# Kernel tuning notes

Measured on AMD Instinct MI355X. Metric: run time of the kernel, lower is better.

Reference implementation:

```python
import jax, jax.numpy as jnp
import numpy as np

N_NODES = 100000
N_EDGES = 1280000
IN_DIM = 64
HID = 64
OUT_DIM = 2
N_GRAPHS = 1000
BN_EPS = 1e-5


def setup_inputs() -> dict:
    key = jax.random.key(0)
    ks = jax.random.split(key, 16)
    x = jax.random.normal(ks[0], (N_NODES, IN_DIM), dtype=jnp.float32)
    edge_index = jax.random.randint(ks[1], (2, N_EDGES), 0, N_NODES, dtype=jnp.int64)
    batch = jnp.sort(jax.random.randint(ks[2], (N_NODES,), 0, N_GRAPHS, dtype=jnp.int64))
    # He-init linear weights (stored as [in, out] so forward is x @ W)
    def he(k, fan_in, fan_out):
        return jax.random.normal(k, (fan_in, fan_out), dtype=jnp.float32) * np.sqrt(2.0 / fan_in)
    return {
        "x": x,
        "edge_index": edge_index,
        "batch": batch,
        "bn_in_g": jnp.ones((IN_DIM,), jnp.float32),
        "bn_in_b": jnp.zeros((IN_DIM,), jnp.float32),
        "W1": he(ks[3], IN_DIM, HID), "b1": jnp.zeros((HID,), jnp.float32),
        "g1": jnp.ones((HID,), jnp.float32), "be1": jnp.zeros((HID,), jnp.float32),
        "W2": he(ks[4], HID, HID), "b2": jnp.zeros((HID,), jnp.float32),
        "g2": jnp.ones((HID,), jnp.float32), "be2": jnp.zeros((HID,), jnp.float32),
        "Wout": he(ks[5], HID, OUT_DIM), "bout": jnp.zeros((OUT_DIM,), jnp.float32),
    }


def _batchnorm(x, g, b):
    # training-mode BN over the node dimension (biased variance, as torch uses for normalization)
    m = jnp.mean(x, axis=0)
    v = jnp.mean(jnp.square(x - m), axis=0)
    return (x - m) * jax.lax.rsqrt(v + BN_EPS) * g + b


def _gcn_norm(edge_index, n):
    # PyG GCNConv normalization with added self-loops:
    # norm_e = deg[src]^-1/2 * deg[dst]^-1/2, deg computed on A + I over targets.
    row = jnp.concatenate([edge_index[0], jnp.arange(n, dtype=edge_index.dtype)])
    col = jnp.concatenate([edge_index[1], jnp.arange(n, dtype=edge_index.dtype)])
    deg = jax.ops.segment_sum(jnp.ones_like(col, dtype=jnp.float32), col, num_segments=n)
    dinv = jnp.where(deg > 0, jax.lax.rsqrt(deg), 0.0)
    norm = dinv[row] * dinv[col]
    return row, col, norm


def _gcn_conv(x, W, b, row, col, norm, n):
    h = x @ W                                   # [N, out]
    msg = h[row] * norm[:, None]                # gather over edges (incl. self-loops)
    agg = jax.ops.segment_sum(msg, col, num_segments=n)
    return agg + b


def reference(x, edge_index, batch, bn_in_g, bn_in_b, W1, b1, g1, be1, W2, b2, g2, be2, Wout, bout):
    n = x.shape[0]
    row, col, norm = _gcn_norm(edge_index, n)
    h = _batchnorm(x, bn_in_g, bn_in_b)         # input BN (dropout = identity in eval)
    h = _gcn_conv(h, W1, b1, row, col, norm, n)
    h = _batchnorm(jax.nn.relu(h), g1, be1)
    h = _gcn_conv(h, W2, b2, row, col, norm, n)
    h = _batchnorm(jax.nn.relu(h), g2, be2)
    # global mean pool per graph
    sums = jax.ops.segment_sum(h, batch, num_segments=N_GRAPHS)
    cnts = jax.ops.segment_sum(jnp.ones((n,), h.dtype), batch, num_segments=N_GRAPHS)
    pooled = sums / jnp.maximum(cnts, 1.0)[:, None]
    return pooled @ Wout + bout                 # [N_GRAPHS, OUT_DIM]
```

## Files before the change

kernel.cpp:

```cpp
#include <hip/hip_runtime.h>
#include <math.h>

#define N_NODES 100000
#define N_EDGES 1280000
#define DIM 64
#define N_GRAPHS 1000
#define BN_EPS 1e-5f
#define NB 392
#define P1B 256
#define P1E 5000
#define SB 400
#define WIN 128
#define NWIN (N_EDGES / WIN)
#define NSLOT 32

__device__ __forceinline__ unsigned int bf16_rtn2(float a, float b) {
    unsigned int ua = __float_as_uint(a);
    unsigned int ub = __float_as_uint(b);
    ua = (ua + 0x7FFFu + ((ua >> 16) & 1u)) >> 16;
    ub = (ub + 0x7FFFu + ((ub >> 16) & 1u)) >> 16;
    return ua | (ub << 16);
}
__device__ __forceinline__ unsigned short bf16r(float a) {
    unsigned int u = __float_as_uint(a);
    return (unsigned short)((u + 0x7FFFu + ((u >> 16) & 1u)) >> 16);
}
__device__ __forceinline__ float bfup(unsigned short u) {
    return __uint_as_float(((unsigned int)u) << 16);
}
__device__ __forceinline__ float blo(unsigned int v) { return __uint_as_float(v << 16); }
__device__ __forceinline__ float bhi(unsigned int v) { return __uint_as_float(v & 0xFFFF0000u); }

__global__ __launch_bounds__(256) void k_p1hist(const int* __restrict__ ei,
                                                const int* __restrict__ batch,
                                                const float* __restrict__ X,
                                                int* __restrict__ bh,
                                                int* __restrict__ start,
                                                float* __restrict__ gsum,
                                                float* __restrict__ gsumsq) {
    int t = threadIdx.x;
    if (blockIdx.x < P1B) {
        __shared__ int hist[NB];
        for (int b = t; b < NB; b += 256) hist[b] = 0;
        __syncthreads();
        int e0 = blockIdx.x * P1E;
        #pragma unroll 4
        for (int e = e0 + t; e < e0 + P1E; e += 256)
            atomicAdd(&hist[ei[N_EDGES + e] >> 8], 1);
        __syncthreads();
        for (int b = t; b < NB; b += 256) bh[b * P1B + blockIdx.x] = hist[b];
    } else if (blockIdx.x < P1B + SB) {
        int grp = blockIdx.x - P1B;
        int j = t & 63, rg = t >> 6;
        int base = grp * 250;
        float s = 0.f, s2 = 0.f;
        for (int i = base + rg; i < base + 250; i += 4) {
            float v = X[i * DIM + j];
            s += v; s2 += v * v;
        }
        __shared__ float ls[256], ls2[256];
        ls[t] = s; ls2[t] = s2;
        __syncthreads();
        if (t < 64) {
            int slot = (grp & (NSLOT - 1)) * DIM;
            s  = ls[j]  + ls[64 + j]  + ls[128 + j]  + ls[192 + j];
            s2 = ls2[j] + ls2[64 + j] + ls2[128 + j] + ls2[192 + j];
            atomicAdd(&gsum[slot + j], s);
            atomicAdd(&gsumsq[slot + j], s2);
        }
    } else {
        int i = (blockIdx.x - P1B - SB) * 256 + t;
        if (i < N_NODES) {
            int cur = batch[i];
            if (i == 0) { for (int q = 0; q <= cur; q++) start[q] = 0; }
            else {
                int prev = batch[i - 1];
                for (int q = prev + 1; q <= cur; q++) start[q] = i;
            }
            if (i == N_NODES - 1)
                for (int q = cur + 1; q <= N_GRAPHS; q++) start[q] = N_NODES;
        }
    }
}

__global__ void k_scan1(const int* __restrict__ bh, int* __restrict__ iscan,
                        int* __restrict__ bsum) {
    __shared__ int ls[256];
    int i = blockIdx.x * 256 + threadIdx.x;
    int v = bh[i];
    ls[threadIdx.x] = v;
    __syncthreads();
    for (int off = 1; off < 256; off <<= 1) {
        int tv = (threadIdx.x >= off) ? ls[threadIdx.x - off] : 0;
        __syncthreads();
        ls[threadIdx.x] += tv;
        __syncthreads();
    }
    iscan[i] = ls[threadIdx.x];
    if (threadIdx.x == 255) bsum[blockIdx.x] = ls[255];
}

__global__ void k_scan2(const int* __restrict__ bsum, int* __restrict__ boff) {
    __shared__ int ls[512];
    int t = threadIdx.x;
    int v0 = (t < NB) ? bsum[t] : 0;
    ls[t] = v0;
    __syncthreads();
    for (int off = 1; off < 512; off <<= 1) {
        int v = (t >= off) ? ls[t - off] : 0;
        __syncthreads();
        ls[t] += v;
        __syncthreads();
    }
    if (t < NB) boff[t] = ls[t] - v0;
}

__global__ __launch_bounds__(256) void k_p1scat(const int* __restrict__ ei,
                                                const int* __restrict__ bh,
                                                const int* __restrict__ iscan,
                                                const int* __restrict__ boff,
                                                int* __restrict__ tmp) {
    __shared__ int cur[NB];
    int blk = blockIdx.x;
    for (int b = threadIdx.x; b < NB; b += 256) {
        int i = b * P1B + blk;
        cur[b] = boff[b] + iscan[i] - bh[i];
    }
    __syncthreads();
    int e0 = blk * P1E;
    for (int e = e0 + threadIdx.x; e < e0 + P1E; e += 256) {
        int r = ei[e], c = ei[N_EDGES + e];
        int pos = atomicAdd(&cur[c >> 8], 1);
        tmp[pos] = (r << 8) | (c & 255);
    }
}

__global__ __launch_bounds__(256) void k_p2a(const int* __restrict__ tmp,
                                             const int* __restrict__ bh,
                                             const int* __restrict__ iscan,
                                             const int* __restrict__ boff,
                                             int* __restrict__ rowstart,
                                             float* __restrict__ dinv,
                                             int* __restrict__ winnode,
                                             float* __restrict__ C) {
    int b = blockIdx.x, t = threadIdx.x;
    int bstart = boff[b] + iscan[b * 256] - bh[b * 256];
    int bend = (b == NB - 1) ? N_EDGES
                             : (boff[b + 1] + iscan[(b + 1) * 256] - bh[(b + 1) * 256]);
    __shared__ int cnt[256], scn[256];
    cnt[t] = 0;
    __syncthreads();
    for (int e = bstart + t; e < bend; e += 256)
        atomicAdd(&cnt[tmp[e] & 255], 1);
    __syncthreads();
    scn[t] = cnt[t];
    __syncthreads();
    for (int off = 1; off < 256; off <<= 1) {
        int v = (t >= off) ? scn[t - off] : 0;
        __syncthreads();
        scn[t] += v;
        __syncthreads();
    }
    int node = b * 256 + t;
    int deg = cnt[t];
    int rs = bstart + scn[t] - deg;
    bool span = false;
    if (node <= N_NODES) rowstart[node] = rs;
    if (node == N_NODES) rowstart[node + 1] = rs;
    if (node < N_NODES) {
        dinv[node] = 1.0f / sqrtf((float)(deg + 1));
        int re = rs + deg;
        for (int w = (rs + WIN - 1) / WIN; w * WIN < re; ++w) winnode[w] = node;
        span = (deg > 0) && (rs / WIN != (re - 1) / WIN);
    }
    int lane = t & 63;
    int wbase = b * 256 + (t & ~63);
    unsigned long long m = __ballot(span);
    while (m) {
        int bit = __builtin_ctzll(m);
        m &= m - 1;
        C[(size_t)(wbase + bit) * DIM + lane] = 0.f;
    }
}

__global__ __launch_bounds__(256) void k_p2b(const int* __restrict__ tmp,
                                             const int* __restrict__ bh,
                                             const int* __restrict__ iscan,
                                             const int* __restrict__ boff,
                                             const int* __restrict__ rowstart,
                                             int* __restrict__ csr) {
    int b = blockIdx.x, t = threadIdx.x;
    int bstart = boff[b] + iscan[b * 256] - bh[b * 256];
    int bend = (b == NB - 1) ? N_EDGES
                             : (boff[b + 1] + iscan[(b + 1) * 256] - bh[(b + 1) * 256]);
    __shared__ int curs[256];
    int node = b * 256 + t;
    curs[t] = (node < N_NODES) ? rowstart[node] : 0;
    __syncthreads();
    for (int e = bstart + t; e < bend; e += 256) {
        int rec = tmp[e];
        int pos = atomicAdd(&curs[rec & 255], 1);
        csr[pos] = (int)((unsigned)rec >> 8);
    }
}

__global__ void k_bnfold(float* __restrict__ gsum, float* __restrict__ gsumsq,
                         const float* __restrict__ g, const float* __restrict__ b,
                         const float* __restrict__ W,
                         float* __restrict__ scale, float* __restrict__ cshift) {
    int j = threadIdx.x;
    float ms = 0.f, m2 = 0.f;
    for (int k = 0; k < NSLOT; k++) {
        ms += gsum[k * DIM + j];   gsum[k * DIM + j] = 0.f;
        m2 += gsumsq[k * DIM + j]; gsumsq[k * DIM + j] = 0.f;
    }
    float mean = ms * (1.0f / N_NODES);
    float var  = m2 * (1.0f / N_NODES) - mean * mean;
    float inv  = 1.0f / sqrtf(var + BN_EPS);
    float sc   = g[j] * inv;
    scale[j] = sc;
    __shared__ float shl[64];
    shl[j] = b[j] - mean * sc;
    __syncthreads();
    float s = 0.f;
    for (int k = 0; k < DIM; k++) s += shl[k] * W[k * DIM + j];
    cshift[j] = s;
}

__global__ void k_bnfinal(const float* __restrict__ gsum, const float* __restrict__ gsumsq,
                          const float* __restrict__ g, const float* __restrict__ b,
                          float* __restrict__ scale, float* __restrict__ shift) {
    int j = threadIdx.x;
    float ms = 0.f, m2 = 0.f;
    for (int k = 0; k < NSLOT; k++) { ms += gsum[k * DIM + j]; m2 += gsumsq[k * DIM + j]; }
    float mean = ms * (1.0f / N_NODES);
    float var  = m2 * (1.0f / N_NODES) - mean * mean;
    float inv  = 1.0f / sqrtf(var + BN_EPS);
    float sc   = g[j] * inv;
    scale[j] = sc;
    shift[j] = b[j] - mean * sc;
}

__global__ __launch_bounds__(256) void k_gemm_f32(const float* __restrict__ X,
                                                  const float* __restrict__ W,
                                                  const float* __restrict__ scale,
                                                  const float* __restrict__ cshift,
                                                  const float* __restrict__ dinv,
                                                  unsigned short* __restrict__ T) {
    __shared__ float Wl[64 * 64];
    __shared__ float Al[64 * 65];
    for (int t = threadIdx.x; t < 4096; t += 256) Wl[t] = W[t] * scale[t >> 6];
    int row0 = blockIdx.x * 64;
    for (int t = threadIdx.x; t < 4096; t += 256) {
        int r = t >> 6, k = t & 63;
        int i = row0 + r;
        Al[r * 65 + k] = (i < N_NODES) ? X[(size_t)i * DIM + k] : 0.f;
    }
    __syncthreads();
    int r = threadIdx.x & 63;
    int q = threadIdx.x >> 6;
    float acc[16];
    #pragma unroll
    for (int jj = 0; jj < 16; jj++) acc[jj] = cshift[q * 16 + jj];
    #pragma unroll 4
    for (int k = 0; k < 64; k++) {
        float a = Al[r * 65 + k];
        const float4* wv = (const float4*)&Wl[k * 64 + q * 16];
        float4 w0 = wv[0], w1 = wv[1], w2 = wv[2], w3 = wv[3];
        acc[0]  += a * w0.x; acc[1]  += a * w0.y; acc[2]  += a * w0.z; acc[3]  += a * w0.w;
        acc[4]  += a * w1.x; acc[5]  += a * w1.y; acc[6]  += a * w1.z; acc[7]  += a * w1.w;
        acc[8]  += a * w2.x; acc[9]  += a * w2.y; acc[10] += a * w2.z; acc[11] += a * w2.w;
        acc[12] += a * w3.x; acc[13] += a * w3.y; acc[14] += a * w3.z; acc[15] += a * w3.w;
    }
    int i = row0 + r;
    if (i < N_NODES) {
        float dv = dinv[i];
        unsigned int pk[8];
        #pragma unroll
        for (int jj = 0; jj < 8; jj++)
            pk[jj] = bf16_rtn2(acc[2 * jj] * dv, acc[2 * jj + 1] * dv);
        uint4* outv = (uint4*)&T[(size_t)i * DIM + q * 16];
        outv[0] = make_uint4(pk[0], pk[1], pk[2], pk[3]);
        outv[1] = make_uint4(pk[4], pk[5], pk[6], pk[7]);
    }
}

__global__ __launch_bounds__(256) void k_gemm_b16(const unsigned short* __restrict__ X,
                                                  const float* __restrict__ W,
                                                  const float* __restrict__ scale,
                                                  const float* __restrict__ cshift,
                                                  const float* __restrict__ dinv,
                                                  unsigned short* __restrict__ T) {
    __shared__ float Wl[64 * 64];
    __shared__ float Al[64 * 65];
    for (int t = threadIdx.x; t < 4096; t += 256) Wl[t] = W[t] * scale[t >> 6];
    int row0 = blockIdx.x * 64;
    for (int t = threadIdx.x; t < 4096; t += 256) {
        int r = t >> 6, k = t & 63;
        int i = row0 + r;
        Al[r * 65 + k] = (i < N_NODES) ? bfup(X[(size_t)i * DIM + k]) : 0.f;
    }
    __syncthreads();
    int r = threadIdx.x & 63;
    int q = threadIdx.x >> 6;
    float acc[16];
    #pragma unroll
    for (int jj = 0; jj < 16; jj++) acc[jj] = cshift[q * 16 + jj];
    #pragma unroll 4
    for (int k = 0; k < 64; k++) {
        float a = Al[r * 65 + k];
        const float4* wv = (const float4*)&Wl[k * 64 + q * 16];
        float4 w0 = wv[0], w1 = wv[1], w2 = wv[2], w3 = wv[3];
        acc[0]  += a * w0.x; acc[1]  += a * w0.y; acc[2]  += a * w0.z; acc[3]  += a * w0.w;
        acc[4]  += a * w1.x; acc[5]  += a * w1.y; acc[6]  += a * w1.z; acc[7]  += a * w1.w;
        acc[8]  += a * w2.x; acc[9]  += a * w2.y; acc[10] += a * w2.z; acc[11] += a * w2.w;
        acc[12] += a * w3.x; acc[13] += a * w3.y; acc[14] += a * w3.z; acc[15] += a * w3.w;
    }
    int i = row0 + r;
    if (i < N_NODES) {
        float dv = dinv[i];
        unsigned int pk[8];
        #pragma unroll
        for (int jj = 0; jj < 8; jj++)
            pk[jj] = bf16_rtn2(acc[2 * jj] * dv, acc[2 * jj + 1] * dv);
        uint4* outv = (uint4*)&T[(size_t)i * DIM + q * 16];
        outv[0] = make_uint4(pk[0], pk[1], pk[2], pk[3]);
        outv[1] = make_uint4(pk[4], pk[5], pk[6], pk[7]);
    }
}


#define SWZ(V, S) __builtin_amdgcn_ds_swizzle((V), (((S) << 5) | 0x10))

#define ISSUE(SRCV, TVV, CV, S0) do {                                 \
    SRCV[0] = SWZ(CV, (S0) + 0); SRCV[1] = SWZ(CV, (S0) + 1);         \
    SRCV[2] = SWZ(CV, (S0) + 2); SRCV[3] = SWZ(CV, (S0) + 3);         \
    TVV[0] = T2[(unsigned)SRCV[0] * 16u + cc];                        \
    TVV[1] = T2[(unsigned)SRCV[1] * 16u + cc];                        \
    TVV[2] = T2[(unsigned)SRCV[2] * 16u + cc];                        \
    TVV[3] = T2[(unsigned)SRCV[3] * 16u + cc];                        \
} while (0)

#define STEP(TVV, U, B, FL) do {                                      \
    const int ebs = e0 + 16 * (B) + 4 * (U);                          \
    uint2 tvv = TVV[U];                                               \
    float a0 = blo(tvv.x), a1 = bhi(tvv.x);                           \
    float a2 = blo(tvv.y), a3 = bhi(tvv.y);                           \
    if (re > ebs + 3) {                                               \
        acc0 += a0; acc1 += a1; acc2 += a2; acc3 += a3;               \
    } else {                                                          \
        int lo = ebs;                                                 \
        while (re <= ebs + 3) {                                       \
            int eg = ebs + gg;                                        \
            if (eg >= lo && eg < re) {                                \
                acc0 += a0; acc1 += a1; acc2 += a2; acc3 += a3;       \
            }                                                         \
            lo = re;                                                  \
            FL();                                                     \
        }                                                             \
        if (ebs + gg >= lo) {                                         \
            acc0 += a0; acc1 += a1; acc2 += a2; acc3 += a3;           \
        }                                                             \
    }                                                                 \
} while (0)

#define CONSUME(TVV, B, FL) do {                                      \
    STEP(TVV, 0, B, FL); STEP(TVV, 1, B, FL);                         \
    STEP(TVV, 2, B, FL); STEP(TVV, 3, B, FL);                         \
} while (0)

#define COMB4()                                                       \
    float t0 = acc0 + __shfl_xor(acc0, 16); t0 += __shfl_xor(t0, 32); \
    float t1 = acc1 + __shfl_xor(acc1, 16); t1 += __shfl_xor(t1, 32); \
    float t2 = acc2 + __shfl_xor(acc2, 16); t2 += __shfl_xor(t2, 32); \
    float t3 = acc3 + __shfl_xor(acc3, 16); t3 += __shfl_xor(t3, 32);

#define REDIST64(OUT, V0, V1, V2, V3)                                 \
    float _r0 = __shfl((V0), lane >> 2);                              \
    float _r1 = __shfl((V1), lane >> 2);                              \
    float _r2 = __shfl((V2), lane >> 2);                              \
    float _r3 = __shfl((V3), lane >> 2);                              \
    float OUT = (lane & 2) ? ((lane & 1) ? _r3 : _r2)                 \
                           : ((lane & 1) ? _r1 : _r0);

#define ADVANCE() do {                                                \
    acc0 = acc1 = acc2 = acc3 = 0.f;                                  \
    ++i; ++k;                                                         \
    if (k < 64) re = __builtin_amdgcn_readlane(rsv, k);               \
    else        re = __builtin_amdgcn_readfirstlane(rowstart[i + 1]); \
    tsv = T2[(unsigned)i * 16u + cc];                                 \
} while (0)

#define FLUSH1() do {                                                 \
    COMB4();                                                          \
    if (part) {                                                       \
        REDIST64(cv, t0, t1, t2, t3);                                 \
        atomicAdd(&C[(size_t)i * DIM + lane], cv);                    \
        part = false;                                                 \
    } else {                                                          \
        int cnt = i - i0;                                             \
        float di;                                                     \
        if (cnt < 64)                                                 \
            di = __int_as_float(                                      \
                __builtin_amdgcn_readlane(__float_as_int(dv), cnt));  \
        else di = dinv[i];                                            \
        float h0 = fmaxf((t0 + blo(tsv.x)) * di + bb.x, 0.f);         \
        float h1 = fmaxf((t1 + bhi(tsv.x)) * di + bb.y, 0.f);         \
        float h2 = fmaxf((t2 + blo(tsv.y)) * di + bb.z, 0.f);         \
        float h3 = fmaxf((t3 + bhi(tsv.y)) * di + bb.w, 0.f);         \
        if (lane < 16)                                                \
            ((uint2*)H)[(unsigned)i * 16u + cc] =                     \
                make_uint2(bf16_rtn2(h0, h1), bf16_rtn2(h2, h3));     \
        s0 += h0; s1 += h1; s2 += h2; s3 += h3;                       \
        q0 += h0 * h0; q1 += h1 * h1; q2 += h2 * h2; q3 += h3 * h3;   \
    }                                                                 \
    ADVANCE();                                                        \
} while (0)

__global__ __launch_bounds__(256) void k_gather1(const unsigned short* __restrict__ T,
                                                 const float* __restrict__ dinv,
                                                 const int* __restrict__ rowstart,
                                                 const int* __restrict__ winnode,
                                                 const int* __restrict__ csr,
                                                 const float* __restrict__ bias,
                                                 float* __restrict__ C,
                                                 unsigned short* __restrict__ H,
                                                 float* __restrict__ gsum,
                                                 float* __restrict__ gsumsq) {
    const int lane = threadIdx.x & 63;
    const int gg = lane >> 4;
    const int cc = lane & 15;
    const int w = blockIdx.x * 4 + (threadIdx.x >> 6);
    const int e0 = w * WIN;
    const int eend = e0 + WIN;
    const uint2* T2 = (const uint2*)T;

    int csrv0 = csr[e0 + 4 * cc + gg];
    int csrv1 = csr[e0 + 64 + 4 * cc + gg];
    int i0 = __builtin_amdgcn_readfirstlane(winnode[w]);
    int rsv = rowstart[min(i0 + lane, N_NODES + 1)];
    float dv = dinv[min(i0 + lane, N_NODES - 1)];
    uint2 tsv = T2[(unsigned)i0 * 16u + cc];
    const float4 bb = ((const float4*)bias)[cc];

    int i = i0, k = 1;
    int re = __builtin_amdgcn_readlane(rsv, 1);
    bool part = __builtin_amdgcn_readlane(rsv, 0) < e0;
    float acc0 = 0.f, acc1 = 0.f, acc2 = 0.f, acc3 = 0.f;
    float s0 = 0.f, s1 = 0.f, s2 = 0.f, s3 = 0.f;
    float q0 = 0.f, q1 = 0.f, q2 = 0.f, q3 = 0.f;

    int srcA[4], srcB[4], srcC[4], srcD[4];
    uint2 tva[4], tvb[4], tvc[4], tvd[4];
    ISSUE(srcA, tva, csrv0, 0);
    ISSUE(srcB, tvb, csrv0, 4);
    ISSUE(srcC, tvc, csrv0, 8);
    ISSUE(srcD, tvd, csrv0, 12);
    CONSUME(tva, 0, FLUSH1);  ISSUE(srcA, tva, csrv1, 0);
    CONSUME(tvb, 1, FLUSH1);  ISSUE(srcB, tvb, csrv1, 4);
    CONSUME(tvc, 2, FLUSH1);  ISSUE(srcC, tvc, csrv1, 8);
    CONSUME(tvd, 3, FLUSH1);  ISSUE(srcD, tvd, csrv1, 12);
    CONSUME(tva, 4, FLUSH1);
    CONSUME(tvb, 5, FLUSH1);
    CONSUME(tvc, 6, FLUSH1);
    CONSUME(tvd, 7, FLUSH1);

    if (part || re > eend) {
        COMB4();
        REDIST64(cv, t0, t1, t2, t3);
        atomicAdd(&C[(size_t)i * DIM + lane], cv);
    } else {
        FLUSH1();
    }

    __shared__ float shs[4][64], shq[4][64];
    int wv = threadIdx.x >> 6;
    if (lane < 16) {
        shs[wv][4 * cc + 0] = s0; shs[wv][4 * cc + 1] = s1;
        shs[wv][4 * cc + 2] = s2; shs[wv][4 * cc + 3] = s3;
        shq[wv][4 * cc + 0] = q0; shq[wv][4 * cc + 1] = q1;
        shq[wv][4 * cc + 2] = q2; shq[wv][4 * cc + 3] = q3;
    }
    __syncthreads();
    if (threadIdx.x < 64) {
        int j = threadIdx.x;
        float vs = shs[0][j] + shs[1][j] + shs[2][j] + shs[3][j];
        float vq = shq[0][j] + shq[1][j] + shq[2][j] + shq[3][j];
        int slot = (blockIdx.x & (NSLOT - 1)) * DIM;
        atomicAdd(&gsum[slot + j], vs);
        atomicAdd(&gsumsq[slot + j], vq);
    }
}

#define FLUSH2() do {                                                 \
    COMB4();                                                          \
    if (part) {                                                       \
        REDIST64(cv, t0, t1, t2, t3);                                 \
        atomicAdd(&C[(size_t)i * DIM + lane], cv);                    \
        part = false;                                                 \
    } else {                                                          \
        int cnt = i - i0;                                             \
        float di;                                                     \
        int gi;                                                       \
        if (cnt < 64) {                                               \
            di = __int_as_float(                                      \
                __builtin_amdgcn_readlane(__float_as_int(dv), cnt));  \
            gi = __builtin_amdgcn_readlane(bv, cnt);                  \
        } else { di = dinv[i]; gi = batch[i]; }                       \
        float h0 = fmaxf((t0 + blo(tsv.x)) * di + bb.x, 0.f);         \
        float h1 = fmaxf((t1 + bhi(tsv.x)) * di + bb.y, 0.f);         \
        float h2 = fmaxf((t2 + blo(tsv.y)) * di + bb.z, 0.f);         \
        float h3 = fmaxf((t3 + bhi(tsv.y)) * di + bb.w, 0.f);         \
        s0 += h0; s1 += h1; s2 += h2; s3 += h3;                       \
        q0 += h0 * h0; q1 += h1 * h1; q2 += h2 * h2; q3 += h3 * h3;   \
        if (gi != cur_g) {                                            \
            if (cur_g >= 0) {                                         \
                REDIST64(pv, ps0, ps1, ps2, ps3);                     \
                atomicAdd(&pool[(size_t)cur_g * DIM + lane], pv);     \
            }                                                         \
            ps0 = ps1 = ps2 = ps3 = 0.f;                              \
            cur_g = gi;                                               \
        }                                                             \
        ps0 += h0; ps1 += h1; ps2 += h2; ps3 += h3;                   \
    }                                                                 \
    ADVANCE();                                                        \
} while (0)

__global__ __launch_bounds__(256) void k_gather2(const unsigned short* __restrict__ T,
                                                 const float* __restrict__ dinv,
                                                 const int* __restrict__ rowstart,
                                                 const int* __restrict__ winnode,
                                                 const int* __restrict__ csr,
                                                 const float* __restrict__ bias,
                                                 const int* __restrict__ batch,
                                                 float* __restrict__ C,
                                                 float* __restrict__ pool,
                                                 float* __restrict__ gsum,
                                                 float* __restrict__ gsumsq) {
    const int lane = threadIdx.x & 63;
    const int gg = lane >> 4;
    const int cc = lane & 15;
    const int w = blockIdx.x * 4 + (threadIdx.x >> 6);
    const int e0 = w * WIN;
    const int eend = e0 + WIN;
    const uint2* T2 = (const uint2*)T;

    int csrv0 = csr[e0 + 4 * cc + gg];
    int csrv1 = csr[e0 + 64 + 4 * cc + gg];
    int i0 = __builtin_amdgcn_readfirstlane(winnode[w]);
    int rsv = rowstart[min(i0 + lane, N_NODES + 1)];
    float dv = dinv[min(i0 + lane, N_NODES - 1)];
    int bv = batch[min(i0 + lane, N_NODES - 1)];
    uint2 tsv = T2[(unsigned)i0 * 16u + cc];
    const float4 bb = ((const float4*)bias)[cc];

    int i = i0, k = 1;
    int re = __builtin_amdgcn_readlane(rsv, 1);
    bool part = __builtin_amdgcn_readlane(rsv, 0) < e0;
    float acc0 = 0.f, acc1 = 0.f, acc2 = 0.f, acc3 = 0.f;
    float s0 = 0.f, s1 = 0.f, s2 = 0.f, s3 = 0.f;
    float q0 = 0.f, q1 = 0.f, q2 = 0.f, q3 = 0.f;
    float ps0 = 0.f, ps1 = 0.f, ps2 = 0.f, ps3 = 0.f;
    int cur_g = -1;

    int srcA[4], srcB[4], srcC[4], srcD[4];
    uint2 tva[4], tvb[4], tvc[4], tvd[4];
    ISSUE(srcA, tva, csrv0, 0);
    ISSUE(srcB, tvb, csrv0, 4);
    ISSUE(srcC, tvc, csrv0, 8);
    ISSUE(srcD, tvd, csrv0, 12);
    CONSUME(tva, 0, FLUSH2);  ISSUE(srcA, tva, csrv1, 0);
    CONSUME(tvb, 1, FLUSH2);  ISSUE(srcB, tvb, csrv1, 4);
    CONSUME(tvc, 2, FLUSH2);  ISSUE(srcC, tvc, csrv1, 8);
    CONSUME(tvd, 3, FLUSH2);  ISSUE(srcD, tvd, csrv1, 12);
    CONSUME(tva, 4, FLUSH2);
    CONSUME(tvb, 5, FLUSH2);
    CONSUME(tvc, 6, FLUSH2);
    CONSUME(tvd, 7, FLUSH2);

    if (part || re > eend) {
        COMB4();
        REDIST64(cv, t0, t1, t2, t3);
        atomicAdd(&C[(size_t)i * DIM + lane], cv);
    } else {
        FLUSH2();
    }
    if (cur_g >= 0) {
        REDIST64(pv, ps0, ps1, ps2, ps3);
        atomicAdd(&pool[(size_t)cur_g * DIM + lane], pv);
    }

    __shared__ float shs[4][64], shq[4][64];
    int wv = threadIdx.x >> 6;
    if (lane < 16) {
        shs[wv][4 * cc + 0] = s0; shs[wv][4 * cc + 1] = s1;
        shs[wv][4 * cc + 2] = s2; shs[wv][4 * cc + 3] = s3;
        shq[wv][4 * cc + 0] = q0; shq[wv][4 * cc + 1] = q1;
        shq[wv][4 * cc + 2] = q2; shq[wv][4 * cc + 3] = q3;
    }
    __syncthreads();
    if (threadIdx.x < 64) {
        int j = threadIdx.x;
        float vs = shs[0][j] + shs[1][j] + shs[2][j] + shs[3][j];
        float vq = shq[0][j] + shq[1][j] + shq[2][j] + shq[3][j];
        int slot = (blockIdx.x & (NSLOT - 1)) * DIM;
        atomicAdd(&gsum[slot + j], vs);
        atomicAdd(&gsumsq[slot + j], vq);
    }
}

__global__ __launch_bounds__(256) void k_strad1(float* __restrict__ C,
                                                const unsigned short* __restrict__ T,
                                                const float* __restrict__ dinv,
                                                const int* __restrict__ rowstart,
                                                const int* __restrict__ winnode,
                                                const float* __restrict__ bias,
                                                unsigned short* __restrict__ H,
                                                float* __restrict__ gsum,
                                                float* __restrict__ gsumsq) {
    int lane = threadIdx.x & 63;
    int wv = threadIdx.x >> 6;
    float bb = bias[lane];
    float s = 0.f, s2 = 0.f;
    __shared__ int anyw;
    if (threadIdx.x == 0) anyw = 0;
    __syncthreads();
    if (blockIdx.x < NWIN / 4) {
        int w = blockIdx.x * 4 + wv;
        int n = winnode[w];
        int rs = rowstart[n];
        if (w == rs / WIN + 1) {
            float di = dinv[n];
            float c = C[(size_t)n * DIM + lane];
            C[(size_t)n * DIM + lane] = 0.f;
            float h = fmaxf((c + bfup(T[(size_t)n * DIM + lane])) * di + bb, 0.f);
            H[(size_t)n * DIM + lane] = bf16r(h);
            s += h; s2 += h * h;
            anyw = 1;
        }
    } else {
        int base = (blockIdx.x - NWIN / 4) * 256 + wv * 64;
        int nb = base + lane;
        int d0 = 0;
        if (nb < N_NODES)
            d0 = (rowstart[nb + 1] == rowstart[nb]) && ((rowstart[nb] & (WIN - 1)) == 0);
        unsigned long long m = __ballot(d0);
        while (m) {
            int b = __builtin_ctzll(m);
            m &= m - 1;
            int n = base + b;
            float di = dinv[n];
            float h = fmaxf(bfup(T[(size_t)n * DIM + lane]) * di + bb, 0.f);
            H[(size_t)n * DIM + lane] = bf16r(h);
            s += h; s2 += h * h;
            anyw = 1;
        }
    }
    __shared__ float ls[256], ls2[256];
    ls[threadIdx.x] = s; ls2[threadIdx.x] = s2;
    __syncthreads();
    if (anyw && threadIdx.x < 64) {
        int j = threadIdx.x;
        int slot = (blockIdx.x & (NSLOT - 1)) * DIM;
        atomicAdd(&gsum[slot + j],   ls[j] + ls[64 + j] + ls[128 + j] + ls[192 + j]);
        atomicAdd(&gsumsq[slot + j], ls2[j] + ls2[64 + j] + ls2[128 + j] + ls2[192 + j]);
    }
}

__global__ __launch_bounds__(256) void k_strad2(const float* __restrict__ C,
                                                const unsigned short* __restrict__ T,
                                                const float* __restrict__ dinv,
                                                const int* __restrict__ rowstart,
                                                const int* __restrict__ winnode,
                                                const float* __restrict__ bias,
                                                const int* __restrict__ batch,
                                                float* __restrict__ pool,
                                                float* __restrict__ gsum,
                                                float* __restrict__ gsumsq) {
    int lane = threadIdx.x & 63;
    int wv = threadIdx.x >> 6;
    float bb = bias[lane];
    float s = 0.f, s2 = 0.f;
    __shared__ int anyw;
    if (threadIdx.x == 0) anyw = 0;
    __syncthreads();
    if (blockIdx.x < NWIN / 4) {
        int w = blockIdx.x * 4 + wv;
        int n = winnode[w];
        int rs = rowstart[n];
        if (w == rs / WIN + 1) {
            float di = dinv[n];
            float h = fmaxf((C[(size_t)n * DIM + lane]
                             + bfup(T[(size_t)n * DIM + lane])) * di + bb, 0.f);
            s += h; s2 += h * h;
            atomicAdd(&pool[(size_t)batch[n] * DIM + lane], h);
            anyw = 1;
        }
    } else {
        int base = (blockIdx.x - NWIN / 4) * 256 + wv * 64;
        int nb = base + lane;
        int d0 = 0;
        if (nb < N_NODES)
            d0 = (rowstart[nb + 1] == rowstart[nb]) && ((rowstart[nb] & (WIN - 1)) == 0);
        unsigned long long m = __ballot(d0);
        while (m) {
            int b = __builtin_ctzll(m);
            m &= m - 1;
            int n = base + b;
            float di = dinv[n];
            float h = fmaxf(bfup(T[(size_t)n * DIM + lane]) * di + bb, 0.f);
            s += h; s2 += h * h;
            atomicAdd(&pool[(size_t)batch[n] * DIM + lane], h);
            anyw = 1;
        }
    }
    __shared__ float ls[256], ls2[256];
    ls[threadIdx.x] = s; ls2[threadIdx.x] = s2;
    __syncthreads();
    if (anyw && threadIdx.x < 64) {
        int j = threadIdx.x;
        int slot = (blockIdx.x & (NSLOT - 1)) * DIM;
        atomicAdd(&gsum[slot + j],   ls[j] + ls[64 + j] + ls[128 + j] + ls[192 + j]);
        atomicAdd(&gsumsq[slot + j], ls2[j] + ls2[64 + j] + ls2[128 + j] + ls2[192 + j]);
    }
}

__global__ void k_final(const float* __restrict__ pool, const int* __restrict__ start,
                        const float* __restrict__ scale, const float* __restrict__ shift,
                        const float* __restrict__ Wout, const float* __restrict__ bout,
                        float* __restrict__ out) {
    int g = blockIdx.x;
    int l = threadIdx.x;
    float c = fmaxf((float)(start[g + 1] - start[g]), 1.f);
    float p = (pool[g * DIM + l] / c) * scale[l] + shift[l];
    float a0 = p * Wout[l * 2 + 0];
    float a1 = p * Wout[l * 2 + 1];
    #pragma unroll
    for (int off = 32; off; off >>= 1) {
        a0 += __shfl_down(a0, off, 64);
        a1 += __shfl_down(a1, off, 64);
    }
    if (l == 0) {
        out[g * 2 + 0] = a0 + bout[0];
        out[g * 2 + 1] = a1 + bout[1];
    }
}

extern "C" void kernel_launch(void* const* d_in, const int* in_sizes, int n_in,
                              void* d_out, int out_size, void* d_ws, size_t ws_size,
                              hipStream_t stream) {
    (void)in_sizes; (void)n_in; (void)out_size; (void)ws_size;
    const float* x       = (const float*)d_in[0];
    const int*   ei      = (const int*)d_in[1];
    const int*   batch   = (const int*)d_in[2];
    const float* bn_in_g = (const float*)d_in[3];
    const float* bn_in_b = (const float*)d_in[4];
    const float* W1      = (const float*)d_in[5];
    const float* b1      = (const float*)d_in[6];
    const float* g1      = (const float*)d_in[7];
    const float* be1     = (const float*)d_in[8];
    const float* W2      = (const float*)d_in[9];
    const float* b2      = (const float*)d_in[10];
    const float* g2      = (const float*)d_in[11];
    const float* be2     = (const float*)d_in[12];
    const float* Wout    = (const float*)d_in[13];
    const float* bout    = (const float*)d_in[14];
    float* out = (float*)d_out;

    char* p = (char*)d_ws;
    float* C = (float*)p;                   p += (size_t)N_NODES * DIM * 4;
    unsigned short* H = (unsigned short*)p; p += (size_t)N_NODES * DIM * 2;
    unsigned short* T = (unsigned short*)p; p += (size_t)N_NODES * DIM * 2;
    int* csr = (int*)p;                     p += (size_t)N_EDGES * 4;
    float* dinv = (float*)p;                p += N_NODES * 4;
    int* bh = (int*)p;                      p += NB * P1B * 4;
    int* iscan = (int*)p;                   p += NB * P1B * 4;
    int* rowstart = (int*)p;                p += (N_NODES + 2) * 4;
    int* winnode = (int*)p;                 p += NWIN * 4;
    int* bsum = (int*)p;                    p += NB * 4;
    int* boff = (int*)p;                    p += NB * 4;
    int* start = (int*)p;                   p += (N_GRAPHS + 2) * 4;
    float* gsum = (float*)p;                p += NSLOT * DIM * 4;
    float* gsumsq = (float*)p;              p += NSLOT * DIM * 4;
    float* scale = (float*)p;               p += DIM * 4;
    float* shift = (float*)p;               p += DIM * 4;
    float* cshift = (float*)p;              p += DIM * 4;
    float* pool = (float*)p;                p += (size_t)N_GRAPHS * DIM * 4;
    int* tmp = (int*)H;

    hipMemsetAsync(gsum, 0, 2 * NSLOT * DIM * sizeof(float), stream);
    hipMemsetAsync(pool, 0, (size_t)N_GRAPHS * DIM * sizeof(float), stream);
    k_p1hist<<<P1B + SB + 392, 256, 0, stream>>>(ei, batch, x, bh, start, gsum, gsumsq);
    k_scan1<<<NB, 256, 0, stream>>>(bh, iscan, bsum);
    k_scan2<<<1, 512, 0, stream>>>(bsum, boff);
    k_p1scat<<<P1B, 256, 0, stream>>>(ei, bh, iscan, boff, tmp);
    k_p2a<<<NB, 256, 0, stream>>>(tmp, bh, iscan, boff, rowstart, dinv, winnode, C);
    k_p2b<<<NB, 256, 0, stream>>>(tmp, bh, iscan, boff, rowstart, csr);

    k_bnfold<<<1, 64, 0, stream>>>(gsum, gsumsq, bn_in_g, bn_in_b, W1, scale, cshift);
    k_gemm_f32<<<(N_NODES + 63) / 64, 256, 0, stream>>>(x, W1, scale, cshift, dinv, T);
    k_gather1<<<NWIN / 4, 256, 0, stream>>>(T, dinv, rowstart, winnode, csr, b1,
                                            C, H, gsum, gsumsq);
    k_strad1<<<NWIN / 4 + 392, 256, 0, stream>>>(C, T, dinv, rowstart, winnode, b1,
                                                 H, gsum, gsumsq);

    k_bnfold<<<1, 64, 0, stream>>>(gsum, gsumsq, g1, be1, W2, scale, cshift);
    k_gemm_b16<<<(N_NODES + 63) / 64, 256, 0, stream>>>(H, W2, scale, cshift, dinv, T);
    k_gather2<<<NWIN / 4, 256, 0, stream>>>(T, dinv, rowstart, winnode, csr, b2,
                                            batch, C, pool, gsum, gsumsq);
    k_strad2<<<NWIN / 4 + 392, 256, 0, stream>>>(C, T, dinv, rowstart, winnode, b2,
                                                 batch, pool, gsum, gsumsq);

    k_bnfinal<<<1, 64, 0, stream>>>(gsum, gsumsq, g2, be2, scale, shift);
    k_final<<<N_GRAPHS, 64, 0, stream>>>(pool, start, scale, shift, Wout, bout, out);
}
```

Before: 317.3 us.

## Fuse small setup kernels and memsets to cut kernel launch count

Removes both memsets and the k_scan2, k_p2b, first k_bnfold and k_bnfinal launches. Their work moves into neighbouring kernels: the input BN fold runs in an extra k_scan1 block, the bucket-offset scan is redone in every k_p1scat and k_p2 block, pool zeroing happens in k_gemm_b16, and the final BN stats are recomputed per block in k_final. Input statistics are written to per-group slots without atomics. The aim is less launch and serialization overhead, paid for with redundant per-block scans and reductions.

```diff
diff --git a/kernel.cpp b/kernel.cpp
--- a/kernel.cpp
+++ b/kernel.cpp
@@ -36,8 +36,8 @@
                                                 const float* __restrict__ X,
                                                 int* __restrict__ bh,
                                                 int* __restrict__ start,
-                                                float* __restrict__ gsum,
-                                                float* __restrict__ gsumsq) {
+                                                float* __restrict__ gs400,
+                                                float* __restrict__ gq400) {
     int t = threadIdx.x;
     if (blockIdx.x < P1B) {
         __shared__ int hist[NB];
@@ -62,11 +62,10 @@
         ls[t] = s; ls2[t] = s2;
         __syncthreads();
         if (t < 64) {
-            int slot = (grp & (NSLOT - 1)) * DIM;
             s  = ls[j]  + ls[64 + j]  + ls[128 + j]  + ls[192 + j];
             s2 = ls2[j] + ls2[64 + j] + ls2[128 + j] + ls2[192 + j];
-            atomicAdd(&gsum[slot + j], s);
-            atomicAdd(&gsumsq[slot + j], s2);
+            gs400[grp * DIM + j] = s;
+            gq400[grp * DIM + j] = s2;
         }
     } else {
         int i = (blockIdx.x - P1B - SB) * 256 + t;
@@ -83,71 +82,115 @@
     }
 }
 
-__global__ void k_scan1(const int* __restrict__ bh, int* __restrict__ iscan,
-                        int* __restrict__ bsum) {
+__global__ __launch_bounds__(256) void k_scan1(const int* __restrict__ bh,
+                                               int* __restrict__ iscan,
+                                               int* __restrict__ bsum,
+                                               const float* __restrict__ gs400,
+                                               const float* __restrict__ gq400,
+                                               const float* __restrict__ bng,
+                                               const float* __restrict__ bnb,
+                                               const float* __restrict__ W1,
+                                               float* __restrict__ scale,
+                                               float* __restrict__ cshift,
+                                               float* __restrict__ gsum32) {
+    int t = threadIdx.x;
+    if (blockIdx.x == NB) {
+        __shared__ float shl[64];
+        if (t < 64) {
+            float ms = 0.f, m2 = 0.f;
+            for (int k2 = 0; k2 < SB; k2++) {
+                ms += gs400[k2 * DIM + t];
+                m2 += gq400[k2 * DIM + t];
+            }
+            float mean = ms * (1.0f / N_NODES);
+            float var  = m2 * (1.0f / N_NODES) - mean * mean;
+            float inv  = 1.0f / sqrtf(var + BN_EPS);
+            float sc   = bng[t] * inv;
+            scale[t] = sc;
+            shl[t] = bnb[t] - mean * sc;
+        }
+        __syncthreads();
+        if (t < 64) {
+            float s = 0.f;
+            for (int k2 = 0; k2 < DIM; k2++) s += shl[k2] * W1[k2 * DIM + t];
+            cshift[t] = s;
+        }
+        for (int z = t; z < 2 * NSLOT * DIM; z += 256) gsum32[z] = 0.f;
+        return;
+    }
     __shared__ int ls[256];
-    int i = blockIdx.x * 256 + threadIdx.x;
+    int i = blockIdx.x * 256 + t;
     int v = bh[i];
-    ls[threadIdx.x] = v;
+    ls[t] = v;
     __syncthreads();
     for (int off = 1; off < 256; off <<= 1) {
-        int tv = (threadIdx.x >= off) ? ls[threadIdx.x - off] : 0;
-        __syncthreads();
-        ls[threadIdx.x] += tv;
-        __syncthreads();
-    }
-    iscan[i] = ls[threadIdx.x];
-    if (threadIdx.x == 255) bsum[blockIdx.x] = ls[255];
-}
-
-__global__ void k_scan2(const int* __restrict__ bsum, int* __restrict__ boff) {
-    __shared__ int ls[512];
-    int t = threadIdx.x;
-    int v0 = (t < NB) ? bsum[t] : 0;
-    ls[t] = v0;
-    __syncthreads();
-    for (int off = 1; off < 512; off <<= 1) {
-        int v = (t >= off) ? ls[t - off] : 0;
-        __syncthreads();
-        ls[t] += v;
-        __syncthreads();
-    }
-    if (t < NB) boff[t] = ls[t] - v0;
+        int tv = (t >= off) ? ls[t - off] : 0;
+        __syncthreads();
+        ls[t] += tv;
+        __syncthreads();
+    }
+    iscan[i] = ls[t];
+    if (t == 255) bsum[blockIdx.x] = ls[255];
 }
 
 __global__ __launch_bounds__(256) void k_p1scat(const int* __restrict__ ei,
                                                 const int* __restrict__ bh,
                                                 const int* __restrict__ iscan,
-                                                const int* __restrict__ boff,
+                                                const int* __restrict__ bsum,
                                                 int* __restrict__ tmp) {
     __shared__ int cur[NB];
-    int blk = blockIdx.x;
-    for (int b = threadIdx.x; b < NB; b += 256) {
+    __shared__ int s0[256], s1[256];
+    int t = threadIdx.x, blk = blockIdx.x;
+    int v0 = bsum[t];
+    int v1 = (t < NB - 256) ? bsum[256 + t] : 0;
+    s0[t] = v0; s1[t] = v1;
+    __syncthreads();
+    for (int off = 1; off < 256; off <<= 1) {
+        int a0 = (t >= off) ? s0[t - off] : 0;
+        int a1 = (t >= off) ? s1[t - off] : 0;
+        __syncthreads();
+        s0[t] += a0; s1[t] += a1;
+        __syncthreads();
+    }
+    int carry = s0[255];
+    {
+        int i = t * P1B + blk;
+        cur[t] = (s0[t] - v0) + iscan[i] - bh[i];
+    }
+    if (t < NB - 256) {
+        int b = 256 + t;
         int i = b * P1B + blk;
-        cur[b] = boff[b] + iscan[i] - bh[i];
+        cur[b] = (carry + s1[t] - v1) + iscan[i] - bh[i];
     }
     __syncthreads();
     int e0 = blk * P1E;
-    for (int e = e0 + threadIdx.x; e < e0 + P1E; e += 256) {
+    for (int e = e0 + t; e < e0 + P1E; e += 256) {
         int r = ei[e], c = ei[N_EDGES + e];
         int pos = atomicAdd(&cur[c >> 8], 1);
         tmp[pos] = (r << 8) | (c & 255);
     }
 }
 
-__global__ __launch_bounds__(256) void k_p2a(const int* __restrict__ tmp,
-                                             const int* __restrict__ bh,
-                                             const int* __restrict__ iscan,
-                                             const int* __restrict__ boff,
-                                             int* __restrict__ rowstart,
-                                             float* __restrict__ dinv,
-                                             int* __restrict__ winnode,
-                                             float* __restrict__ C) {
+__global__ __launch_bounds__(256) void k_p2(const int* __restrict__ tmp,
+                                            const int* __restrict__ bsum,
+                                            int* __restrict__ rowstart,
+                                            float* __restrict__ dinv,
+                                            int* __restrict__ winnode,
+                                            float* __restrict__ C,
+                                            int* __restrict__ csr) {
     int b = blockIdx.x, t = threadIdx.x;
-    int bstart = boff[b] + iscan[b * 256] - bh[b * 256];
-    int bend = (b == NB - 1) ? N_EDGES
-                             : (boff[b + 1] + iscan[(b + 1) * 256] - bh[(b + 1) * 256]);
-    __shared__ int cnt[256], scn[256];
+    __shared__ int red[256];
+    int part = 0;
+    for (int k2 = t; k2 < b; k2 += 256) part += bsum[k2];
+    red[t] = part;
+    __syncthreads();
+    for (int off = 128; off; off >>= 1) {
+        if (t < off) red[t] += red[t + off];
+        __syncthreads();
+    }
+    int bstart = red[0];
+    int bend = bstart + bsum[b];
+    __shared__ int cnt[256], scn[256], curs[256];
     cnt[t] = 0;
     __syncthreads();
     for (int e = bstart + t; e < bend; e += 256)
@@ -181,21 +224,7 @@
         m &= m - 1;
         C[(size_t)(wbase + bit) * DIM + lane] = 0.f;
     }
-}
-
-__global__ __launch_bounds__(256) void k_p2b(const int* __restrict__ tmp,
-                                             const int* __restrict__ bh,
-                                             const int* __restrict__ iscan,
-                                             const int* __restrict__ boff,
-                                             const int* __restrict__ rowstart,
-                                             int* __restrict__ csr) {
-    int b = blockIdx.x, t = threadIdx.x;
-    int bstart = boff[b] + iscan[b * 256] - bh[b * 256];
-    int bend = (b == NB - 1) ? N_EDGES
-                             : (boff[b + 1] + iscan[(b + 1) * 256] - bh[(b + 1) * 256]);
-    __shared__ int curs[256];
-    int node = b * 256 + t;
-    curs[t] = (node < N_NODES) ? rowstart[node] : 0;
+    curs[t] = rs;
     __syncthreads();
     for (int e = bstart + t; e < bend; e += 256) {
         int rec = tmp[e];
@@ -225,20 +254,6 @@
     float s = 0.f;
     for (int k = 0; k < DIM; k++) s += shl[k] * W[k * DIM + j];
     cshift[j] = s;
-}
-
-__global__ void k_bnfinal(const float* __restrict__ gsum, const float* __restrict__ gsumsq,
-                          const float* __restrict__ g, const float* __restrict__ b,
-                          float* __restrict__ scale, float* __restrict__ shift) {
-    int j = threadIdx.x;
-    float ms = 0.f, m2 = 0.f;
-    for (int k = 0; k < NSLOT; k++) { ms += gsum[k * DIM + j]; m2 += gsumsq[k * DIM + j]; }
-    float mean = ms * (1.0f / N_NODES);
-    float var  = m2 * (1.0f / N_NODES) - mean * mean;
-    float inv  = 1.0f / sqrtf(var + BN_EPS);
-    float sc   = g[j] * inv;
-    scale[j] = sc;
-    shift[j] = b[j] - mean * sc;
 }
 
 __global__ __launch_bounds__(256) void k_gemm_f32(const float* __restrict__ X,
@@ -290,7 +305,10 @@
                                                   const float* __restrict__ scale,
                                                   const float* __restrict__ cshift,
                                                   const float* __restrict__ dinv,
-                                                  unsigned short* __restrict__ T) {
+                                                  unsigned short* __restrict__ T,
+                                                  float* __restrict__ pool) {
+    if (blockIdx.x < N_GRAPHS && threadIdx.x < 64)
+        pool[(size_t)blockIdx.x * DIM + threadIdx.x] = 0.f;
     __shared__ float Wl[64 * 64];
     __shared__ float Al[64 * 65];
     for (int t = threadIdx.x; t < 4096; t += 256) Wl[t] = W[t] * scale[t >> 6];
@@ -328,7 +346,6 @@
         outv[1] = make_uint4(pk[4], pk[5], pk[6], pk[7]);
     }
 }
-
 
 #define SWZ(V, S) __builtin_amdgcn_ds_swizzle((V), (((S) << 5) | 0x10))
 
@@ -726,13 +743,21 @@
 }
 
 __global__ void k_final(const float* __restrict__ pool, const int* __restrict__ start,
-                        const float* __restrict__ scale, const float* __restrict__ shift,
+                        const float* __restrict__ gsum, const float* __restrict__ gsumsq,
+                        const float* __restrict__ g, const float* __restrict__ be,
                         const float* __restrict__ Wout, const float* __restrict__ bout,
                         float* __restrict__ out) {
-    int g = blockIdx.x;
+    int gr = blockIdx.x;
     int l = threadIdx.x;
-    float c = fmaxf((float)(start[g + 1] - start[g]), 1.f);
-    float p = (pool[g * DIM + l] / c) * scale[l] + shift[l];
+    float ms = 0.f, m2 = 0.f;
+    for (int k = 0; k < NSLOT; k++) { ms += gsum[k * DIM + l]; m2 += gsumsq[k * DIM + l]; }
+    float mean = ms * (1.0f / N_NODES);
+    float var  = m2 * (1.0f / N_NODES) - mean * mean;
+    float inv  = 1.0f / sqrtf(var + BN_EPS);
+    float sc   = g[l] * inv;
+    float sh   = be[l] - mean * sc;
+    float c = fmaxf((float)(start[gr + 1] - start[gr]), 1.f);
+    float p = (pool[gr * DIM + l] / c) * sc + sh;
     float a0 = p * Wout[l * 2 + 0];
     float a1 = p * Wout[l * 2 + 1];
     #pragma unroll
@@ -741,8 +766,8 @@
         a1 += __shfl_down(a1, off, 64);
     }
     if (l == 0) {
-        out[g * 2 + 0] = a0 + bout[0];
-        out[g * 2 + 1] = a1 + bout[1];
+        out[gr * 2 + 0] = a0 + bout[0];
+        out[gr * 2 + 1] = a1 + bout[1];
     }
 }
 
@@ -778,39 +803,36 @@
     int* rowstart = (int*)p;                p += (N_NODES + 2) * 4;
     int* winnode = (int*)p;                 p += NWIN * 4;
     int* bsum = (int*)p;                    p += NB * 4;
-    int* boff = (int*)p;                    p += NB * 4;
     int* start = (int*)p;                   p += (N_GRAPHS + 2) * 4;
-    float* gsum = (float*)p;                p += NSLOT * DIM * 4;
-    float* gsumsq = (float*)p;              p += NSLOT * DIM * 4;
+    float* gsum32 = (float*)p;              p += NSLOT * DIM * 4;
+    float* gsumsq32 = (float*)p;            p += NSLOT * DIM * 4;
+    float* gs400 = (float*)p;               p += (size_t)SB * DIM * 4;
+    float* gq400 = (float*)p;               p += (size_t)SB * DIM * 4;
     float* scale = (float*)p;               p += DIM * 4;
-    float* shift = (float*)p;               p += DIM * 4;
     float* cshift = (float*)p;              p += DIM * 4;
     float* pool = (float*)p;                p += (size_t)N_GRAPHS * DIM * 4;
     int* tmp = (int*)H;
 
-    hipMemsetAsync(gsum, 0, 2 * NSLOT * DIM * sizeof(float), stream);
-    hipMemsetAsync(pool, 0, (size_t)N_GRAPHS * DIM * sizeof(float), stream);
-    k_p1hist<<<P1B + SB + 392, 256, 0, stream>>>(ei, batch, x, bh, start, gsum, gsumsq);
-    k_scan1<<<NB, 256, 0, stream>>>(bh, iscan, bsum);
-    k_scan2<<<1, 512, 0, stream>>>(bsum, boff);
-    k_p1scat<<<P1B, 256, 0, stream>>>(ei, bh, iscan, boff, tmp);
-    k_p2a<<<NB, 256, 0, stream>>>(tmp, bh, iscan, boff, rowstart, dinv, winnode, C);
-    k_p2b<<<NB, 256, 0, stream>>>(tmp, bh, iscan, boff, rowstart, csr);
-
-    k_bnfold<<<1, 64, 0, stream>>>(gsum, gsumsq, bn_in_g, bn_in_b, W1, scale, cshift);
+    k_p1hist<<<P1B + SB + 392, 256, 0, stream>>>(ei, batch, x, bh, start, gs400, gq400);
+    k_scan1<<<NB + 1, 256, 0, stream>>>(bh, iscan, bsum, gs400, gq400,
+                                        bn_in_g, bn_in_b, W1, scale, cshift, gsum32);
+    k_p1scat<<<P1B, 256, 0, stream>>>(ei, bh, iscan, bsum, tmp);
+    k_p2<<<NB, 256, 0, stream>>>(tmp, bsum, rowstart, dinv, winnode, C, csr);
+
     k_gemm_f32<<<(N_NODES + 63) / 64, 256, 0, stream>>>(x, W1, scale, cshift, dinv, T);
     k_gather1<<<NWIN / 4, 256, 0, stream>>>(T, dinv, rowstart, winnode, csr, b1,
-                                            C, H, gsum, gsumsq);
+                                            C, H, gsum32, gsumsq32);
     k_strad1<<<NWIN / 4 + 392, 256, 0, stream>>>(C, T, dinv, rowstart, winnode, b1,
-                                                 H, gsum, gsumsq);
-
-    k_bnfold<<<1, 64, 0, stream>>>(gsum, gsumsq, g1, be1, W2, scale, cshift);
-    k_gemm_b16<<<(N_NODES + 63) / 64, 256, 0, stream>>>(H, W2, scale, cshift, dinv, T);
+                                                 H, gsum32, gsumsq32);
+
+    k_bnfold<<<1, 64, 0, stream>>>(gsum32, gsumsq32, g1, be1, W2, scale, cshift);
+    k_gemm_b16<<<(N_NODES + 63) / 64, 256, 0, stream>>>(H, W2, scale, cshift, dinv, T,
+                                                        pool);
     k_gather2<<<NWIN / 4, 256, 0, stream>>>(T, dinv, rowstart, winnode, csr, b2,
-                                            batch, C, pool, gsum, gsumsq);
+                                            batch, C, pool, gsum32, gsumsq32);
     k_strad2<<<NWIN / 4 + 392, 256, 0, stream>>>(C, T, dinv, rowstart, winnode, b2,
-                                                 batch, pool, gsum, gsumsq);
-
-    k_bnfinal<<<1, 64, 0, stream>>>(gsum, gsumsq, g2, be2, scale, shift);
-    k_final<<<N_GRAPHS, 64, 0, stream>>>(pool, start, scale, shift, Wout, bout, out);
-}
+                                                 batch, pool, gsum32, gsumsq32);
+
+    k_final<<<N_GRAPHS, 64, 0, stream>>>(pool, start, gsum32, gsumsq32, g2, be2,
+                                         Wout, bout, out);
+}
```

New measurement: 312.7 us. No clear change (-1.5%).
